# Kernel optimization log

Measured on AMD Instinct MI355X. Metric: run time of the kernel, lower is better.

## Reference

```python
import jax, jax.numpy as jnp
import numpy as np

N, E, B = 16000, 256000, 64
H = 4
DIMS = [960, 512, 256, 128]  # per-layer input dims; output dim of layer i is DIMS[i+1] = HID[i]*H
HID = [128, 64, 32]


def setup_inputs() -> dict:
    key = jax.random.key(0)
    ks = jax.random.split(key, 16)
    inp = {}
    inp["x"] = jax.random.normal(ks[0], (N, DIMS[0]), jnp.float32)
    inp["edge_index"] = jax.random.randint(ks[1], (2, E), 0, N)
    inp["batch"] = jnp.sort(jax.random.randint(ks[2], (N,), 0, B))
    k = 3
    for i in range(3):
        din, c = DIMS[i], HID[i]
        s = 1.0 / np.sqrt(din).astype(np.float32)
        inp[f"Wl{i+1}"] = jax.random.normal(ks[k], (din, H * c), jnp.float32) * s; k += 1
        inp[f"Wr{i+1}"] = jax.random.normal(ks[k], (din, H * c), jnp.float32) * s; k += 1
        inp[f"att{i+1}"] = jax.random.normal(ks[k], (H, c), jnp.float32) * (1.0 / np.sqrt(c).astype(np.float32)); k += 1
        inp[f"b{i+1}"] = jnp.zeros((H * c,), jnp.float32)
        inp[f"gnw{i+1}"] = jnp.ones((H * c,), jnp.float32)
        inp[f"gnb{i+1}"] = jnp.zeros((H * c,), jnp.float32)
        inp[f"gnm{i+1}"] = jnp.ones((H * c,), jnp.float32)
    d = DIMS[-1]
    inp["aW1"] = jax.random.normal(ks[k], (d, 128), jnp.float32) * (1.0 / np.sqrt(d).astype(np.float32)); k += 1
    inp["ab1"] = jnp.zeros((128,), jnp.float32)
    inp["aW2"] = jax.random.normal(ks[k], (128, 1), jnp.float32) * (1.0 / np.sqrt(128).astype(np.float32)); k += 1
    inp["ab2"] = jnp.zeros((1,), jnp.float32)
    return inp


def _gatv2(x, src, dst, Wl, Wr, att, bias):
    # PyG GATv2Conv, concat=True, negative_slope=0.2 (self-loops already in src/dst)
    n = x.shape[0]
    h, c = att.shape
    xl = (x @ Wl).reshape(n, h, c)
    xr = (x @ Wr).reshape(n, h, c)
    e = jax.nn.leaky_relu(xl[src] + xr[dst], negative_slope=0.2)  # [E,H,C]
    logit = jnp.einsum('ehc,hc->eh', e, att)                      # [E,H]
    m = jax.ops.segment_max(logit, dst, num_segments=n)
    m = jnp.nan_to_num(m, neginf=0.0)
    p = jnp.exp(logit - m[dst])
    z = jax.ops.segment_sum(p, dst, num_segments=n)
    alpha = p / (z[dst] + 1e-16)                                  # segment softmax over dst
    out = jax.ops.segment_sum(alpha[:, :, None] * xl[src], dst, num_segments=n)
    return out.reshape(n, h * c) + bias


def _graphnorm(x, w, b, ms, eps=1e-5):
    # PyG GraphNorm with batch=None: normalize over all nodes as one graph
    mean = jnp.mean(x, axis=0, keepdims=True)
    xc = x - ms * mean
    var = jnp.mean(xc * xc, axis=0, keepdims=True)
    return w * xc / jnp.sqrt(var + eps) + b


def reference(x, edge_index, batch,
              Wl1, Wr1, att1, b1, gnw1, gnb1, gnm1,
              Wl2, Wr2, att2, b2, gnw2, gnb2, gnm2,
              Wl3, Wr3, att3, b3, gnw3, gnb3, gnm3,
              aW1, ab1, aW2, ab2):
    n = x.shape[0]
    loop = jnp.arange(n)
    src = jnp.concatenate([edge_index[0], loop])  # add self-loops (PyG default)
    dst = jnp.concatenate([edge_index[1], loop])
    layers = [(Wl1, Wr1, att1, b1, gnw1, gnb1, gnm1),
              (Wl2, Wr2, att2, b2, gnw2, gnb2, gnm2),
              (Wl3, Wr3, att3, b3, gnw3, gnb3, gnm3)]
    for Wl, Wr, att, bb, gw, gb, gm in layers:
        x = _gatv2(x, src, dst, Wl, Wr, att, bb)
        x = _graphnorm(x, gw, gb, gm)
        x = jax.nn.relu(x)
    # AttentionalAggregation pooling: gate MLP -> segment softmax over graphs -> weighted sum
    gate = jax.nn.relu(x @ aW1 + ab1) @ aW2 + ab2  # [N,1]
    mg = jax.ops.segment_max(gate, batch, num_segments=B)
    mg = jnp.nan_to_num(mg, neginf=0.0)
    pg = jnp.exp(gate - mg[batch])
    zg = jax.ops.segment_sum(pg, batch, num_segments=B)
    a = pg / (zg[batch] + 1e-16)
    return jax.ops.segment_sum(a * x, batch, num_segments=B)  # [B, 128]
```

## Files before the change

kernel.cpp:

```cpp
#include <hip/hip_runtime.h>
#include <cstdint>
#include <cstddef>
#include <math.h>


typedef _Float16  h16x8  __attribute__((ext_vector_type(8)));
typedef _Float16  h16x4  __attribute__((ext_vector_type(4)));
typedef _Float16  h16x2  __attribute__((ext_vector_type(2)));
typedef float     f32x4  __attribute__((ext_vector_type(4)));

template<int R> struct HV;
template<> struct HV<8> { using T = h16x8; };
template<> struct HV<4> { using T = h16x4; };
template<> struct HV<2> { using T = h16x2; };

__device__ __forceinline__ void gload_lds16(const void* g, void* l) {
    __builtin_amdgcn_global_load_lds(
        (const __attribute__((address_space(1))) uint32_t*)g,
        (__attribute__((address_space(3))) uint32_t*)l, 16, 0, 0);
}

__device__ __forceinline__ int swz_k(int k, int row) {
    return (k & ~31) | ((((k >> 3) & 3) ^ ((row >> 1) & 3)) << 3) | (k & 7);
}

__device__ __forceinline__ void conv_elem(int t, const float* __restrict__ Wl,
                                          const float* __restrict__ Wr,
                                          _Float16* __restrict__ Wt, int K, int HC) {
    int k = t / HC, n = t - k * HC;
    const int ks = swz_k(k, n);
    Wt[(size_t)n * K + ks] = (_Float16)Wl[t];
    if (Wr) Wt[(size_t)(HC + n) * K + ks] = (_Float16)Wr[t];
}

__global__ __launch_bounds__(256) void conv_all(
        const float* __restrict__ Wl0, const float* __restrict__ Wr0, _Float16* __restrict__ T0,
        const float* __restrict__ Wl1, const float* __restrict__ Wr1, _Float16* __restrict__ T1,
        const float* __restrict__ Wl2, const float* __restrict__ Wr2, _Float16* __restrict__ T2,
        const float* __restrict__ Wa, _Float16* __restrict__ Ta) {
    int t = blockIdx.x * blockDim.x + threadIdx.x;
    if (t < 491520) { conv_elem(t, Wl0, Wr0, T0, 960, 512); return; }
    t -= 491520;
    if (t < 131072) { conv_elem(t, Wl1, Wr1, T1, 512, 256); return; }
    t -= 131072;
    if (t < 32768)  { conv_elem(t, Wl2, Wr2, T2, 256, 128); return; }
    t -= 32768;
    if (t < 16384)  conv_elem(t, Wa, nullptr, Ta, 128, 128);
}

template<bool NORM>
__global__ __launch_bounds__(256) void prep_a(
        const float* __restrict__ X, const float* __restrict__ alp,
        const float* __restrict__ bet, _Float16* __restrict__ Out,
        int M, int K) {
    int t = blockIdx.x * blockDim.x + threadIdx.x;
    const int gpr = K >> 3;
    if (t >= M * gpr) return;
    int m = t / gpr, g = t - m * gpr;
    int k = g << 3;
    const float* src = X + (size_t)m * K + k;
    float4 u0 = *(const float4*)src;
    float4 u1 = *(const float4*)(src + 4);
    float uu[8] = {u0.x, u0.y, u0.z, u0.w, u1.x, u1.y, u1.z, u1.w};
    if (NORM) {
        float4 a0 = *(const float4*)(alp + k);
        float4 a1 = *(const float4*)(alp + k + 4);
        float4 b0 = *(const float4*)(bet + k);
        float4 b1 = *(const float4*)(bet + k + 4);
        float aa[8] = {a0.x, a0.y, a0.z, a0.w, a1.x, a1.y, a1.z, a1.w};
        float bb[8] = {b0.x, b0.y, b0.z, b0.w, b1.x, b1.y, b1.z, b1.w};
        #pragma unroll
        for (int j = 0; j < 8; ++j) uu[j] = fmaxf(aa[j] * uu[j] + bb[j], 0.f);
    }
    h16x8 h;
    #pragma unroll
    for (int j = 0; j < 8; ++j) h[j] = (_Float16)uu[j];
    *(h16x8*)&Out[(size_t)m * K + swz_k(k, m)] = h;
}

template<bool BIAS, bool RELU, typename OutT>
__global__ __launch_bounds__(256) void mfma_gemm(
        const _Float16* __restrict__ A, const _Float16* __restrict__ Bt,
        const float* __restrict__ bias, OutT* __restrict__ C,
        int M, int K, int N) {
    __shared__ __attribute__((aligned(16))) _Float16 sA[2][128 * 32];
    __shared__ __attribute__((aligned(16))) _Float16 sB[2][128 * 32];

    const int gx  = gridDim.x;
    const int nwg = gx * gridDim.y;
    const int id  = blockIdx.y * gx + blockIdx.x;
    const int q   = nwg >> 3, r = nwg & 7;
    const int xcd = id & 7, sub = id >> 3;
    const int nid = (xcd < r) ? (xcd * (q + 1) + sub)
                              : (r * (q + 1) + (xcd - r) * q + sub);
    const int row0 = (nid / gx) * 128;
    const int col0 = (nid % gx) * 128;

    const int tid  = threadIdx.x;
    const int lane = tid & 63;
    const int w    = tid >> 6;
    const int wm   = w >> 1, wn = w & 1;
    const int lr   = lane & 15, lg = lane >> 4;
    const int bRow = w * 16 + (lane >> 2);
    const int bGrp = (lane & 3) * 8;
    const int fGrp = (lg ^ ((lr >> 1) & 3)) * 8;

    f32x4 acc[4][4] = {};

    const _Float16* pa = A  + (size_t)(row0 + bRow) * K + bGrp;
    const _Float16* pb = Bt + (size_t)(col0 + bRow) * K + bGrp;

    auto stage = [&](int buf, int k0) {
        gload_lds16(pa + k0,                  (char*)&sA[buf][0] + w * 1024);
        gload_lds16(pa + (size_t)64 * K + k0, (char*)&sA[buf][0] + 4096 + w * 1024);
        gload_lds16(pb + k0,                  (char*)&sB[buf][0] + w * 1024);
        gload_lds16(pb + (size_t)64 * K + k0, (char*)&sB[buf][0] + 4096 + w * 1024);
    };

    stage(0, 0);
    __syncthreads();
    int cur = 0;
    for (int k0 = 0; k0 < K; k0 += 32) {
        if (k0 + 32 < K) stage(cur ^ 1, k0 + 32);
        h16x8 ah[4], bh[4];
        #pragma unroll
        for (int i = 0; i < 4; ++i) {
            ah[i] = *(const h16x8*)&sA[cur][(wm * 64 + i * 16 + lr) * 32 + fGrp];
            bh[i] = *(const h16x8*)&sB[cur][(wn * 64 + i * 16 + lr) * 32 + fGrp];
        }
        #pragma unroll
        for (int i = 0; i < 4; ++i)
            #pragma unroll
            for (int j = 0; j < 4; ++j)
                acc[i][j] = __builtin_amdgcn_mfma_f32_16x16x32_f16(ah[i], bh[j], acc[i][j], 0, 0, 0);
        __syncthreads();
        cur ^= 1;
    }

    #pragma unroll
    for (int i = 0; i < 4; ++i) {
        const int rowb = row0 + wm * 64 + i * 16 + lg * 4;
        #pragma unroll
        for (int j = 0; j < 4; ++j) {
            const int col = col0 + wn * 64 + j * 16 + lr;
            const float bv = BIAS ? bias[col] : 0.f;
            #pragma unroll
            for (int qq = 0; qq < 4; ++qq) {
                float v = acc[i][j][qq] + bv;
                if (RELU) v = fmaxf(v, 0.f);
                C[(size_t)(rowb + qq) * N + col] = (OutT)v;
            }
        }
    }
}

__global__ void csr_count(const int* __restrict__ edst, int E, int Etot,
                          int* __restrict__ deg) {
    int e = blockIdx.x * blockDim.x + threadIdx.x;
    if (e >= Etot) return;
    int d = (e < E) ? edst[e] : e - E;
    atomicAdd(&deg[d], 1);
}

__global__ __launch_bounds__(1024) void scan_deg(const int* __restrict__ deg,
                                                 int* __restrict__ row_start,
                                                 int* __restrict__ cursor, int N) {
    __shared__ int part[1024];
    const int tid = threadIdx.x;
    const int base = tid * 16;
    int loc[16];
    int s = 0;
    #pragma unroll
    for (int j = 0; j < 16; ++j) {
        int i = base + j;
        s += (i < N) ? deg[i] : 0;
        loc[j] = s;
    }
    part[tid] = s; __syncthreads();
    #pragma unroll
    for (int off = 1; off < 1024; off <<= 1) {
        int t2 = (tid >= off) ? part[tid - off] : 0;
        __syncthreads();
        part[tid] += t2;
        __syncthreads();
    }
    const int pre = tid ? part[tid - 1] : 0;
    #pragma unroll
    for (int j = 0; j < 16; ++j) {
        int i = base + j;
        if (i < N) {
            int st = pre + (j ? loc[j - 1] : 0);
            row_start[i] = st;
            cursor[i]    = st;
            if (i == N - 1) row_start[N] = pre + loc[j];
        }
    }
}

__global__ void csr_fill(const int* __restrict__ esrc, const int* __restrict__ edst,
                         int E, int Etot, int* __restrict__ cursor,
                         int* __restrict__ src_perm) {
    int e = blockIdx.x * blockDim.x + threadIdx.x;
    if (e >= Etot) return;
    int s, d;
    if (e < E) { s = esrc[e]; d = edst[e]; }
    else       { s = d = e - E; }
    int pos = atomicAdd(&cursor[d], 1);
    src_perm[pos] = s;
}

template<int LOG2C>
__global__ __launch_bounds__(256) void gat_agg(
        const _Float16* __restrict__ xlr,
        const float* __restrict__ att, const float* __restrict__ bias,
        const int* __restrict__ row_start, const int* __restrict__ src_perm,
        int N, float* __restrict__ out) {
    constexpr int HC  = 4 << LOG2C;
    constexpr int R   = HC / 64;
    constexpr int STR = 2 * HC;
    constexpr int U   = 8;
    using hvec = typename HV<R>::T;

    const int widx = threadIdx.x >> 6;
    const int lane = threadIdx.x & 63;
    const int dst  = blockIdx.x * 4 + widx;
    if (dst >= N) return;

    const int base = lane * R;
    float xrv[R], attv[R], acc[R];
    {
        hvec xv = *(const hvec*)&xlr[(size_t)dst * STR + HC + base];
        #pragma unroll
        for (int it = 0; it < R; ++it) {
            xrv[it]  = (float)xv[it];
            attv[it] = att[base + it];
            acc[it]  = 0.f;
        }
    }

    float z = 0.f;
    const int start = row_start[dst], end = row_start[dst + 1];

    int cs = start;
    for (; cs + U <= end; cs += U) {
        hvec rows[U];
        #pragma unroll
        for (int k = 0; k < U; ++k) {
            int src = __builtin_amdgcn_readfirstlane(src_perm[cs + k]);
            rows[k] = *(const hvec*)&xlr[(size_t)src * STR + base];
        }
        #pragma unroll
        for (int k = 0; k < U; ++k) {
            float rf[R], a = 0.f;
            #pragma unroll
            for (int it = 0; it < R; ++it) {
                rf[it] = (float)rows[k][it];
                float v = rf[it] + xrv[it];
                v = v > 0.f ? v : 0.2f * v;
                a += v * attv[it];
            }
            #pragma unroll
            for (int s = 1; s < 16; s <<= 1) a += __shfl_xor(a, s);
            float p = __expf(a);
            z += p;
            #pragma unroll
            for (int it = 0; it < R; ++it) acc[it] += p * rf[it];
        }
    }
    for (; cs < end; ++cs) {
        int src = __builtin_amdgcn_readfirstlane(src_perm[cs]);
        hvec row = *(const hvec*)&xlr[(size_t)src * STR + base];
        float rf[R], a = 0.f;
        #pragma unroll
        for (int it = 0; it < R; ++it) {
            rf[it] = (float)row[it];
            float v = rf[it] + xrv[it];
            v = v > 0.f ? v : 0.2f * v;
            a += v * attv[it];
        }
        #pragma unroll
        for (int s = 1; s < 16; s <<= 1) a += __shfl_xor(a, s);
        float p = __expf(a);
        z += p;
        #pragma unroll
        for (int it = 0; it < R; ++it) acc[it] += p * rf[it];
    }

    const float inv = 1.f / (z + 1e-16f);
    float ov[R];
    #pragma unroll
    for (int it = 0; it < R; ++it) ov[it] = acc[it] * inv + bias[base + it];
    float* po = out + (size_t)dst * HC + base;
    if constexpr (R == 8) {
        *(float4*)po       = make_float4(ov[0], ov[1], ov[2], ov[3]);
        *(float4*)(po + 4) = make_float4(ov[4], ov[5], ov[6], ov[7]);
    } else if constexpr (R == 4) {
        *(float4*)po = make_float4(ov[0], ov[1], ov[2], ov[3]);
    } else {
        *(float2*)po = make_float2(ov[0], ov[1]);
    }
}

__global__ __launch_bounds__(64) void colstats(const float* __restrict__ x, int HC,
                                               float* __restrict__ s1, float* __restrict__ s2) {
    int c  = blockIdx.x * 64 + threadIdx.x;
    int r0 = blockIdx.y * 128;
    float a = 0.f, b = 0.f;
    for (int r = r0; r < r0 + 128; ++r) {
        float v = x[(size_t)r * HC + c];
        a += v; b += v * v;
    }
    atomicAdd(&s1[c], a);
    atomicAdd(&s2[c], b);
}

__global__ void gn_finalize(const float* __restrict__ s1, const float* __restrict__ s2,
                            const float* __restrict__ w, const float* __restrict__ b,
                            const float* __restrict__ ms, int HC, float invN,
                            float* __restrict__ alpha, float* __restrict__ beta) {
    int c = blockIdx.x * blockDim.x + threadIdx.x;
    if (c >= HC) return;
    float mean = s1[c] * invN;
    float ex2  = s2[c] * invN;
    float a    = ms[c] * mean;
    float var  = ex2 - 2.f * a * mean + a * a;
    float al   = w[c] * rsqrtf(var + 1e-5f);
    alpha[c] = al;
    beta[c]  = b[c] - a * al;
}

__global__ __launch_bounds__(256) void gate_dot(const float* __restrict__ hid,
                                                const float* __restrict__ aW2,
                                                const float* __restrict__ ab2,
                                                float* __restrict__ gate, int N) {
    int w = (blockIdx.x * blockDim.x + threadIdx.x) >> 6;
    if (w >= N) return;
    int lane = threadIdx.x & 63;
    const float* ph = hid + (size_t)w * 128;
    float a = ph[lane] * aW2[lane] + ph[lane + 64] * aW2[lane + 64];
    #pragma unroll
    for (int s = 32; s; s >>= 1) a += __shfl_xor(a, s);
    if (lane == 0) gate[w] = a + ab2[0];
}

__global__ __launch_bounds__(1024) void attn_pool(const float* __restrict__ x,
                                                  const float* __restrict__ alpha,
                                                  const float* __restrict__ beta,
                                                  const float* __restrict__ gate,
                                                  const int* __restrict__ batch,
                                                  int N, float* __restrict__ out) {
    const int b   = blockIdx.x;
    const int tid = threadIdx.x;
    const int grp = tid >> 7;
    const int ch  = tid & 127;
    int lo, hi;
    { int l = 0, r = N; while (l < r) { int mid = (l + r) >> 1; if (batch[mid] < b) l = mid + 1; else r = mid; } lo = l; }
    { int l = lo, r = N; while (l < r) { int mid = (l + r) >> 1; if (batch[mid] < b + 1) l = mid + 1; else r = mid; } hi = l; }
    if (lo >= hi) { if (tid < 128) out[b * 128 + tid] = 0.f; return; }

    __shared__ float red[1024];
    float mx = -INFINITY;
    for (int n = lo + tid; n < hi; n += 1024) mx = fmaxf(mx, gate[n]);
    red[tid] = mx; __syncthreads();
    for (int s = 512; s; s >>= 1) { if (tid < s) red[tid] = fmaxf(red[tid], red[tid + s]); __syncthreads(); }
    mx = red[0]; __syncthreads();
    float zs = 0.f;
    for (int n = lo + tid; n < hi; n += 1024) zs += __expf(gate[n] - mx);
    red[tid] = zs; __syncthreads();
    for (int s = 512; s; s >>= 1) { if (tid < s) red[tid] += red[tid + s]; __syncthreads(); }
    zs = red[0]; __syncthreads();
    const float alc = alpha[ch], bec = beta[ch];
    float acc = 0.f;
    for (int n = lo + grp; n < hi; n += 8) {
        float wv = __expf(gate[n] - mx);
        float v  = fmaxf(alc * x[(size_t)n * 128 + ch] + bec, 0.f);
        acc += wv * v;
    }
    red[tid] = acc; __syncthreads();
    if (tid < 128) {
        float s = red[tid];
        #pragma unroll
        for (int g = 1; g < 8; ++g) s += red[g * 128 + tid];
        out[b * 128 + tid] = s / (zs + 1e-16f);
    }
}

extern "C" void kernel_launch(void* const* d_in, const int* in_sizes, int n_in,
                              void* d_out, int out_size, void* d_ws, size_t ws_size,
                              hipStream_t stream) {
    const float* x0  = (const float*)d_in[0];
    const int* edge  = (const int*)d_in[1];
    const int* batch = (const int*)d_in[2];
    const int N = in_sizes[2];
    const int E = in_sizes[1] / 2;
    const int Etot = E + N;
    const int dims[4] = {960, 512, 256, 128};

    const float* Wl[3]   = {(const float*)d_in[3],  (const float*)d_in[10], (const float*)d_in[17]};
    const float* Wr[3]   = {(const float*)d_in[4],  (const float*)d_in[11], (const float*)d_in[18]};
    const float* attp[3] = {(const float*)d_in[5],  (const float*)d_in[12], (const float*)d_in[19]};
    const float* bi[3]   = {(const float*)d_in[6],  (const float*)d_in[13], (const float*)d_in[20]};
    const float* gw[3]   = {(const float*)d_in[7],  (const float*)d_in[14], (const float*)d_in[21]};
    const float* gb[3]   = {(const float*)d_in[8],  (const float*)d_in[15], (const float*)d_in[22]};
    const float* gm[3]   = {(const float*)d_in[9],  (const float*)d_in[16], (const float*)d_in[23]};
    const float* aW1 = (const float*)d_in[24];
    const float* ab1 = (const float*)d_in[25];
    const float* aW2 = (const float*)d_in[26];
    const float* ab2 = (const float*)d_in[27];

    size_t off = 0;
    auto alloc = [&](size_t bytes) -> char* {
        char* p = (char*)d_ws + off;
        off += (bytes + 255) & ~(size_t)255;
        return p;
    };
    _Float16* xlr     = (_Float16*)alloc((size_t)N * 1024 * 2);
    _Float16* aT      = (_Float16*)alloc((size_t)N * 960 * 2);
    float*   bufC     = (float*)alloc((size_t)N * 512 * 4);
    int*     deg      = (int*)alloc((size_t)N * 4);
    int*     row_start= (int*)alloc((size_t)(N + 1) * 4);
    int*     cursor   = (int*)alloc((size_t)N * 4);
    int*     src_perm = (int*)alloc((size_t)Etot * 4);
    float*   s12      = (float*)alloc(3 * 1024 * 4);
    float*   alB      = (float*)alloc(3 * 512 * 4);
    float*   beB      = (float*)alloc(3 * 512 * 4);
    float*   gateB    = (float*)alloc((size_t)N * 4);
    _Float16* wt[3];
    for (int l = 0; l < 3; ++l)
        wt[l] = (_Float16*)alloc((size_t)dims[l] * (2 * dims[l + 1]) * 2);
    _Float16* awt = (_Float16*)alloc(128 * 128 * 2);
    float* poolhid = (float*)xlr;
    (void)ws_size; (void)n_in; (void)out_size;

    conv_all<<<(671744 + 255) / 256, 256, 0, stream>>>(
        Wl[0], Wr[0], wt[0], Wl[1], Wr[1], wt[1], Wl[2], Wr[2], wt[2], aW1, awt);

    hipMemsetAsync(deg, 0, (size_t)N * sizeof(int), stream);
    hipMemsetAsync(s12, 0, 3 * 1024 * sizeof(float), stream);
    csr_count<<<(Etot + 255) / 256, 256, 0, stream>>>(edge + E, E, Etot, deg);
    scan_deg<<<1, 1024, 0, stream>>>(deg, row_start, cursor, N);
    csr_fill<<<(Etot + 255) / 256, 256, 0, stream>>>(edge, edge + E, E, Etot,
                                                     cursor, src_perm);

    for (int l = 0; l < 3; ++l) {
        const int K = dims[l], HC = dims[l + 1];
        const int ngrp = N * (K >> 3);
        if (l == 0)
            prep_a<false><<<(ngrp + 255) / 256, 256, 0, stream>>>(
                x0, nullptr, nullptr, aT, N, K);
        else
            prep_a<true><<<(ngrp + 255) / 256, 256, 0, stream>>>(
                bufC, alB + (l - 1) * 512, beB + (l - 1) * 512, aT, N, K);

        dim3 ggrid((2 * HC) / 128, N / 128);
        mfma_gemm<false, false, _Float16><<<ggrid, 256, 0, stream>>>(
            aT, wt[l], nullptr, xlr, N, K, 2 * HC);

        const int agrid = (N + 3) / 4;
        if (l == 0)      gat_agg<7><<<agrid, 256, 0, stream>>>(xlr, attp[l], bi[l], row_start, src_perm, N, bufC);
        else if (l == 1) gat_agg<6><<<agrid, 256, 0, stream>>>(xlr, attp[l], bi[l], row_start, src_perm, N, bufC);
        else             gat_agg<5><<<agrid, 256, 0, stream>>>(xlr, attp[l], bi[l], row_start, src_perm, N, bufC);

        colstats<<<dim3(HC / 64, N / 128), 64, 0, stream>>>(bufC, HC, s12 + l * 1024, s12 + l * 1024 + 512);
        gn_finalize<<<(HC + 63) / 64, 64, 0, stream>>>(s12 + l * 1024, s12 + l * 1024 + 512,
                                                       gw[l], gb[l], gm[l], HC, 1.0f / N,
                                                       alB + l * 512, beB + l * 512);
    }

    prep_a<true><<<(N * 16 + 255) / 256, 256, 0, stream>>>(
        bufC, alB + 1024, beB + 1024, aT, N, 128);
    mfma_gemm<true, true, float><<<dim3(1, N / 128), 256, 0, stream>>>(
        aT, awt, ab1, poolhid, N, 128, 128);
    gate_dot<<<(N * 64 + 255) / 256, 256, 0, stream>>>(poolhid, aW2, ab2, gateB, N);
    attn_pool<<<64, 1024, 0, stream>>>(bufC, alB + 1024, beB + 1024, gateB, batch, N, (float*)d_out);
}
```

Baseline: 354.1 us.

## Split layer-1 GAT aggregation across two waves and fuse gate dot into GEMM

The layer-1 aggregation now splits each destination's 512 channels over two wavefronts, which doubles the number of waves in flight and halves per-lane register width. The edge prefetch changes from fixed blocks of 8 to one predicated batch of up to 24 neighbours, followed by a scalar tail loop. The pooling gate's second linear layer is fused into the MFMA GEMM epilogue through shuffle and LDS atomic reductions, removing the hidden-activation store and the separate gate_dot kernel. The costs are duplicated xr/att loads across the split waves and extra register pressure from the 24-row prefetch.

```diff
diff --git a/kernel.cpp b/kernel.cpp
--- a/kernel.cpp
+++ b/kernel.cpp
@@ -78,13 +78,16 @@
     *(h16x8*)&Out[(size_t)m * K + swz_k(k, m)] = h;
 }
 
-template<bool BIAS, bool RELU, typename OutT>
+template<bool BIAS, bool RELU, bool GATE, typename OutT>
 __global__ __launch_bounds__(256) void mfma_gemm(
         const _Float16* __restrict__ A, const _Float16* __restrict__ Bt,
         const float* __restrict__ bias, OutT* __restrict__ C,
-        int M, int K, int N) {
+        int M, int K, int N,
+        const float* __restrict__ gw2, const float* __restrict__ gb2,
+        float* __restrict__ gate) {
     __shared__ __attribute__((aligned(16))) _Float16 sA[2][128 * 32];
     __shared__ __attribute__((aligned(16))) _Float16 sB[2][128 * 32];
+    __shared__ float gsum[128];
 
     const int gx  = gridDim.x;
     const int nwg = gx * gridDim.y;
@@ -118,6 +121,7 @@
     };
 
     stage(0, 0);
+    if (GATE) { if (tid < 128) gsum[tid] = 0.f; }
     __syncthreads();
     int cur = 0;
     for (int k0 = 0; k0 < K; k0 += 32) {
@@ -137,20 +141,52 @@
         cur ^= 1;
     }
 
-    #pragma unroll
-    for (int i = 0; i < 4; ++i) {
-        const int rowb = row0 + wm * 64 + i * 16 + lg * 4;
-        #pragma unroll
-        for (int j = 0; j < 4; ++j) {
-            const int col = col0 + wn * 64 + j * 16 + lr;
-            const float bv = BIAS ? bias[col] : 0.f;
+    if constexpr (!GATE) {
+        #pragma unroll
+        for (int i = 0; i < 4; ++i) {
+            const int rowb = row0 + wm * 64 + i * 16 + lg * 4;
+            #pragma unroll
+            for (int j = 0; j < 4; ++j) {
+                const int col = col0 + wn * 64 + j * 16 + lr;
+                const float bv = BIAS ? bias[col] : 0.f;
+                #pragma unroll
+                for (int qq = 0; qq < 4; ++qq) {
+                    float v = acc[i][j][qq] + bv;
+                    if (RELU) v = fmaxf(v, 0.f);
+                    C[(size_t)(rowb + qq) * N + col] = (OutT)v;
+                }
+            }
+        }
+    } else {
+        float gp[4][4] = {};
+        float w2[4];
+        #pragma unroll
+        for (int j = 0; j < 4; ++j) w2[j] = gw2[wn * 64 + j * 16 + lr];
+        #pragma unroll
+        for (int i = 0; i < 4; ++i)
+            #pragma unroll
+            for (int j = 0; j < 4; ++j) {
+                const int col = wn * 64 + j * 16 + lr;
+                const float bv = bias[col];
+                #pragma unroll
+                for (int qq = 0; qq < 4; ++qq) {
+                    float v = fmaxf(acc[i][j][qq] + bv, 0.f);
+                    gp[i][qq] += v * w2[j];
+                }
+            }
+        #pragma unroll
+        for (int i = 0; i < 4; ++i)
             #pragma unroll
             for (int qq = 0; qq < 4; ++qq) {
-                float v = acc[i][j][qq] + bv;
-                if (RELU) v = fmaxf(v, 0.f);
-                C[(size_t)(rowb + qq) * N + col] = (OutT)v;
+                float p = gp[i][qq];
+                p += __shfl_xor(p, 1);
+                p += __shfl_xor(p, 2);
+                p += __shfl_xor(p, 4);
+                p += __shfl_xor(p, 8);
+                if (lr == 0) atomicAdd(&gsum[wm * 64 + i * 16 + lg * 4 + qq], p);
             }
-        }
+        __syncthreads();
+        if (tid < 128) gate[row0 + tid] = gsum[tid] + gb2[0];
     }
 }
 
@@ -209,24 +245,27 @@
     src_perm[pos] = s;
 }
 
-template<int LOG2C>
+template<int LOG2C, int SPLIT, int U>
 __global__ __launch_bounds__(256) void gat_agg(
         const _Float16* __restrict__ xlr,
         const float* __restrict__ att, const float* __restrict__ bias,
         const int* __restrict__ row_start, const int* __restrict__ src_perm,
         int N, float* __restrict__ out) {
     constexpr int HC  = 4 << LOG2C;
-    constexpr int R   = HC / 64;
+    constexpr int CW  = HC / SPLIT;
+    constexpr int R   = CW / 64;
+    constexpr int LH  = 16 * SPLIT;
     constexpr int STR = 2 * HC;
-    constexpr int U   = 8;
     using hvec = typename HV<R>::T;
 
     const int widx = threadIdx.x >> 6;
     const int lane = threadIdx.x & 63;
-    const int dst  = blockIdx.x * 4 + widx;
+    const int v    = blockIdx.x * 4 + widx;
+    const int dst  = v / SPLIT;
+    const int part = v - dst * SPLIT;
     if (dst >= N) return;
 
-    const int base = lane * R;
+    const int base = part * CW + lane * R;
     float xrv[R], attv[R], acc[R];
     {
         hvec xv = *(const hvec*)&xlr[(size_t)dst * STR + HC + base];
@@ -238,48 +277,50 @@
         }
     }
 
+    const int start = row_start[dst], end = row_start[dst + 1];
+    const int nb = min(U, end - start);
     float z = 0.f;
-    const int start = row_start[dst], end = row_start[dst + 1];
-
-    int cs = start;
-    for (; cs + U <= end; cs += U) {
-        hvec rows[U];
-        #pragma unroll
-        for (int k = 0; k < U; ++k) {
-            int src = __builtin_amdgcn_readfirstlane(src_perm[cs + k]);
+
+    hvec rows[U];
+    #pragma unroll
+    for (int k = 0; k < U; ++k) {
+        if (k < nb) {
+            int src = __builtin_amdgcn_readfirstlane(src_perm[start + k]);
             rows[k] = *(const hvec*)&xlr[(size_t)src * STR + base];
         }
-        #pragma unroll
-        for (int k = 0; k < U; ++k) {
+    }
+    #pragma unroll
+    for (int k = 0; k < U; ++k) {
+        if (k < nb) {
             float rf[R], a = 0.f;
             #pragma unroll
             for (int it = 0; it < R; ++it) {
                 rf[it] = (float)rows[k][it];
-                float v = rf[it] + xrv[it];
-                v = v > 0.f ? v : 0.2f * v;
-                a += v * attv[it];
+                float vv = rf[it] + xrv[it];
+                vv = vv > 0.f ? vv : 0.2f * vv;
+                a += vv * attv[it];
             }
             #pragma unroll
-            for (int s = 1; s < 16; s <<= 1) a += __shfl_xor(a, s);
+            for (int s = 1; s < LH; s <<= 1) a += __shfl_xor(a, s);
             float p = __expf(a);
             z += p;
             #pragma unroll
             for (int it = 0; it < R; ++it) acc[it] += p * rf[it];
         }
     }
-    for (; cs < end; ++cs) {
+    for (int cs = start + U; cs < end; ++cs) {
         int src = __builtin_amdgcn_readfirstlane(src_perm[cs]);
         hvec row = *(const hvec*)&xlr[(size_t)src * STR + base];
         float rf[R], a = 0.f;
         #pragma unroll
         for (int it = 0; it < R; ++it) {
             rf[it] = (float)row[it];
-            float v = rf[it] + xrv[it];
-            v = v > 0.f ? v : 0.2f * v;
-            a += v * attv[it];
-        }
-        #pragma unroll
-        for (int s = 1; s < 16; s <<= 1) a += __shfl_xor(a, s);
+            float vv = rf[it] + xrv[it];
+            vv = vv > 0.f ? vv : 0.2f * vv;
+            a += vv * attv[it];
+        }
+        #pragma unroll
+        for (int s = 1; s < LH; s <<= 1) a += __shfl_xor(a, s);
         float p = __expf(a);
         z += p;
         #pragma unroll
@@ -327,20 +368,6 @@
     float al   = w[c] * rsqrtf(var + 1e-5f);
     alpha[c] = al;
     beta[c]  = b[c] - a * al;
-}
-
-__global__ __launch_bounds__(256) void gate_dot(const float* __restrict__ hid,
-                                                const float* __restrict__ aW2,
-                                                const float* __restrict__ ab2,
-                                                float* __restrict__ gate, int N) {
-    int w = (blockIdx.x * blockDim.x + threadIdx.x) >> 6;
-    if (w >= N) return;
-    int lane = threadIdx.x & 63;
-    const float* ph = hid + (size_t)w * 128;
-    float a = ph[lane] * aW2[lane] + ph[lane + 64] * aW2[lane + 64];
-    #pragma unroll
-    for (int s = 32; s; s >>= 1) a += __shfl_xor(a, s);
-    if (lane == 0) gate[w] = a + ab2[0];
 }
 
 __global__ __launch_bounds__(1024) void attn_pool(const float* __restrict__ x,
@@ -429,7 +456,6 @@
     for (int l = 0; l < 3; ++l)
         wt[l] = (_Float16*)alloc((size_t)dims[l] * (2 * dims[l + 1]) * 2);
     _Float16* awt = (_Float16*)alloc(128 * 128 * 2);
-    float* poolhid = (float*)xlr;
     (void)ws_size; (void)n_in; (void)out_size;
 
     conv_all<<<(671744 + 255) / 256, 256, 0, stream>>>(
@@ -453,13 +479,12 @@
                 bufC, alB + (l - 1) * 512, beB + (l - 1) * 512, aT, N, K);
 
         dim3 ggrid((2 * HC) / 128, N / 128);
-        mfma_gemm<false, false, _Float16><<<ggrid, 256, 0, stream>>>(
-            aT, wt[l], nullptr, xlr, N, K, 2 * HC);
-
-        const int agrid = (N + 3) / 4;
-        if (l == 0)      gat_agg<7><<<agrid, 256, 0, stream>>>(xlr, attp[l], bi[l], row_start, src_perm, N, bufC);
-        else if (l == 1) gat_agg<6><<<agrid, 256, 0, stream>>>(xlr, attp[l], bi[l], row_start, src_perm, N, bufC);
-        else             gat_agg<5><<<agrid, 256, 0, stream>>>(xlr, attp[l], bi[l], row_start, src_perm, N, bufC);
+        mfma_gemm<false, false, false, _Float16><<<ggrid, 256, 0, stream>>>(
+            aT, wt[l], nullptr, xlr, N, K, 2 * HC, nullptr, nullptr, nullptr);
+
+        if (l == 0)      gat_agg<7, 2, 24><<<(N * 2 + 3) / 4, 256, 0, stream>>>(xlr, attp[l], bi[l], row_start, src_perm, N, bufC);
+        else if (l == 1) gat_agg<6, 1, 24><<<(N + 3) / 4, 256, 0, stream>>>(xlr, attp[l], bi[l], row_start, src_perm, N, bufC);
+        else             gat_agg<5, 1, 24><<<(N + 3) / 4, 256, 0, stream>>>(xlr, attp[l], bi[l], row_start, src_perm, N, bufC);
 
         colstats<<<dim3(HC / 64, N / 128), 64, 0, stream>>>(bufC, HC, s12 + l * 1024, s12 + l * 1024 + 512);
         gn_finalize<<<(HC + 63) / 64, 64, 0, stream>>>(s12 + l * 1024, s12 + l * 1024 + 512,
@@ -469,8 +494,7 @@
 
     prep_a<true><<<(N * 16 + 255) / 256, 256, 0, stream>>>(
         bufC, alB + 1024, beB + 1024, aT, N, 128);
-    mfma_gemm<true, true, float><<<dim3(1, N / 128), 256, 0, stream>>>(
-        aT, awt, ab1, poolhid, N, 128, 128);
-    gate_dot<<<(N * 64 + 255) / 256, 256, 0, stream>>>(poolhid, aW2, ab2, gateB, N);
+    mfma_gemm<true, true, true, float><<<dim3(1, N / 128), 256, 0, stream>>>(
+        aT, awt, ab1, nullptr, N, 128, 128, aW2, ab2, gateB);
     attn_pool<<<64, 1024, 0, stream>>>(bufC, alB + 1024, beB + 1024, gateB, batch, N, (float*)d_out);
 }
```

Result: slower. 416.0 us (+17.5%).
